# Kernel tuning notes

Hardware: AMD Instinct MI355X
Metric: run time of the kernel (lower is better)

The kernel has to match this reference:

```python
import jax, jax.numpy as jnp
import numpy as np

B, M_IN, M_OUT, C = 4, 16, 32, 32


def setup_inputs() -> dict:
    key = jax.random.key(0)
    kx, = jax.random.split(key, 1)
    x = jax.random.normal(kx, (B, M_IN, C, C, C, C), dtype=jnp.float32)
    init = jnp.ones((M_IN, M_OUT), dtype=jnp.float32) / M_IN
    return {"x": x, "alpha": init, "beta": init, "gamma": init, "delta": init}


def reference(x, alpha, beta, gamma, delta):
    # Faithful to the torch code's permute+sum bookkeeping (note: torch's
    # permute(0,1,3,2,4,5).sum((2,4,5)) reduces ORIGINAL axes (3,4,5),
    # keeping original axis 2 -- identical to s1).
    s1 = x.sum(axis=(3, 4, 5))  # (B, M_in, C), keeps axis 2
    s2 = x.sum(axis=(3, 4, 5))  # same as s1 (permuted-sum in torch keeps axis 2)
    s3 = x.sum(axis=(2, 4, 5))  # keeps axis 3
    s4 = x.sum(axis=(2, 3, 5))  # keeps axis 4
    s = jnp.stack([s1, s2, s3, s4], axis=2)            # (B, M_in, 4, C)
    w = jnp.stack([alpha, beta, gamma, delta], axis=2)  # (M_in, M_out, 4)
    # 'bmic,mnd->bnic': sums over m and w's stack axis d; keeps s's stack axis i.
    out = jnp.einsum('bmic,mnd->bnic', s, w)            # (B, M_out, 4, C)
    return out
```

## Files before the change

kernel.cpp:

```cpp
#include <hip/hip_runtime.h>


__global__ __launch_bounds__(256) void zero_k(float* __restrict__ ws) {
    int i = blockIdx.x * 256 + threadIdx.x;
    if (i < 6144) ws[i] = 0.0f;
}

__global__ __launch_bounds__(256) void reduce_k(const float* __restrict__ x,
                                                float* __restrict__ ws) {
    const int t   = threadIdx.x;
    const int bid = blockIdx.x;
    const int bm  = bid >> 5;
    const int lane = t & 63;
    const int wv   = t >> 6;

    __shared__ float lds3[4][32];
    __shared__ float lds4[32];
    __shared__ float lds1[4];

    const float4* xv = (const float4*)x + (size_t)bid * 8192;

    float total = 0.0f;
    #pragma unroll
    for (int it = 0; it < 32; ++it) {
        float4 v = xv[it * 256 + t];
        float s = (v.x + v.y) + (v.z + v.w);
        total += s;
        #pragma unroll
        for (int off = 1; off < 64; off <<= 1)
            s += __shfl_xor(s, off, 64);
        if (lane == 0) lds3[wv][it] = s;
    }

    float g = total;
    g += __shfl_xor(g, 1, 64);
    g += __shfl_xor(g, 2, 64);
    g += __shfl_xor(g, 4, 64);
    if ((t & 7) == 0) lds4[t >> 3] = g;

    float wsum = g;
    wsum += __shfl_xor(wsum, 8, 64);
    wsum += __shfl_xor(wsum, 16, 64);
    wsum += __shfl_xor(wsum, 32, 64);
    if (lane == 0) lds1[wv] = wsum;

    __syncthreads();

    float* s1 = ws;
    float* s3 = ws + 2048;
    float* s4 = ws + 4096;
    if (t < 32) {
        float v3 = lds3[0][t] + lds3[1][t] + lds3[2][t] + lds3[3][t];
        atomicAdd(&s3[bm * 32 + t], v3);
        atomicAdd(&s4[bm * 32 + t], lds4[t]);
    }
    if (t == 0) {
        s1[bid] = lds1[0] + lds1[1] + lds1[2] + lds1[3];
    }
}

__global__ __launch_bounds__(256) void finalize_k(const float* __restrict__ ws,
                                                  const float* __restrict__ alpha,
                                                  const float* __restrict__ beta,
                                                  const float* __restrict__ gamma,
                                                  const float* __restrict__ delta,
                                                  float* __restrict__ out) {
    __shared__ float W[512];
    const int t = threadIdx.x;
    #pragma unroll
    for (int i = t; i < 512; i += 256)
        W[i] = alpha[i] + beta[i] + gamma[i] + delta[i];
    __syncthreads();

    int gid = blockIdx.x * 256 + t;
    int c  = gid & 31;
    int i4 = (gid >> 5) & 3;
    int n  = (gid >> 7) & 31;
    int b  = gid >> 12;

    const float* s = ws + (i4 <= 1 ? 0 : (i4 == 2 ? 2048 : 4096));
    float acc = 0.0f;
    #pragma unroll
    for (int m = 0; m < 16; ++m)
        acc += s[(b * 16 + m) * 32 + c] * W[m * 32 + n];
    out[gid] = acc;
}

extern "C" void kernel_launch(void* const* d_in, const int* in_sizes, int n_in,
                              void* d_out, int out_size, void* d_ws, size_t ws_size,
                              hipStream_t stream) {
    const float* x     = (const float*)d_in[0];
    const float* alpha = (const float*)d_in[1];
    const float* beta  = (const float*)d_in[2];
    const float* gamma = (const float*)d_in[3];
    const float* delta = (const float*)d_in[4];
    float* out = (float*)d_out;
    float* ws  = (float*)d_ws;

    zero_k<<<24, 256, 0, stream>>>(ws);
    reduce_k<<<2048, 256, 0, stream>>>(x, ws);
    finalize_k<<<64, 256, 0, stream>>>(ws, alpha, beta, gamma, delta, out);
}
```

Baseline: 364.8 us.

## Replace atomics and zero kernel with per-block partials reduced in finalize

The reduce kernel now writes per-block partial sums for s3 and s4 to workspace instead of using atomicAdd into zeroed buffers, so the zeroing kernel launch goes away. The per-lane shuffle tree is cut to three steps, with partials staged through a padded LDS tile. s1 is rebuilt in finalize from the s3 partials. The finalize kernel now runs only 4 blocks that each reduce 32 partials per entry before the contraction, so that final step has much less parallelism.

```diff
diff --git a/kernel.cpp b/kernel.cpp
--- a/kernel.cpp
+++ b/kernel.cpp
@@ -1,89 +1,94 @@
 #include <hip/hip_runtime.h>
 
 
-__global__ __launch_bounds__(256) void zero_k(float* __restrict__ ws) {
-    int i = blockIdx.x * 256 + threadIdx.x;
-    if (i < 6144) ws[i] = 0.0f;
-}
-
 __global__ __launch_bounds__(256) void reduce_k(const float* __restrict__ x,
-                                                float* __restrict__ ws) {
+                                                float* __restrict__ s3part,
+                                                float* __restrict__ s4part) {
     const int t   = threadIdx.x;
     const int bid = blockIdx.x;
-    const int bm  = bid >> 5;
-    const int lane = t & 63;
-    const int wv   = t >> 6;
+    const int wv  = t >> 6;
+    const int g   = (t & 63) >> 3;
 
-    __shared__ float lds3[4][32];
-    __shared__ float lds4[32];
-    __shared__ float lds1[4];
+    __shared__ float lds3[32][33];
 
     const float4* xv = (const float4*)x + (size_t)bid * 8192;
 
-    float total = 0.0f;
-    #pragma unroll
+    float acc4 = 0.0f;
+    #pragma unroll 4
     for (int it = 0; it < 32; ++it) {
         float4 v = xv[it * 256 + t];
         float s = (v.x + v.y) + (v.z + v.w);
-        total += s;
-        #pragma unroll
-        for (int off = 1; off < 64; off <<= 1)
-            s += __shfl_xor(s, off, 64);
-        if (lane == 0) lds3[wv][it] = s;
+        s += __shfl_xor(s, 1, 64);
+        s += __shfl_xor(s, 2, 64);
+        s += __shfl_xor(s, 4, 64);
+        acc4 += s;
+        if ((t & 7) == 0) lds3[it][wv * 8 + g] = s;
     }
 
-    float g = total;
-    g += __shfl_xor(g, 1, 64);
-    g += __shfl_xor(g, 2, 64);
-    g += __shfl_xor(g, 4, 64);
-    if ((t & 7) == 0) lds4[t >> 3] = g;
-
-    float wsum = g;
-    wsum += __shfl_xor(wsum, 8, 64);
-    wsum += __shfl_xor(wsum, 16, 64);
-    wsum += __shfl_xor(wsum, 32, 64);
-    if (lane == 0) lds1[wv] = wsum;
+    if ((t & 7) == 0) s4part[bid * 32 + (t >> 3)] = acc4;
 
     __syncthreads();
 
-    float* s1 = ws;
-    float* s3 = ws + 2048;
-    float* s4 = ws + 4096;
     if (t < 32) {
-        float v3 = lds3[0][t] + lds3[1][t] + lds3[2][t] + lds3[3][t];
-        atomicAdd(&s3[bm * 32 + t], v3);
-        atomicAdd(&s4[bm * 32 + t], lds4[t]);
-    }
-    if (t == 0) {
-        s1[bid] = lds1[0] + lds1[1] + lds1[2] + lds1[3];
+        float a = 0.0f;
+        #pragma unroll
+        for (int k = 0; k < 32; ++k) a += lds3[t][k];
+        s3part[bid * 32 + t] = a;
     }
 }
 
-__global__ __launch_bounds__(256) void finalize_k(const float* __restrict__ ws,
+__global__ __launch_bounds__(256) void finalize_k(const float* __restrict__ s3part,
+                                                  const float* __restrict__ s4part,
                                                   const float* __restrict__ alpha,
                                                   const float* __restrict__ beta,
                                                   const float* __restrict__ gamma,
                                                   const float* __restrict__ delta,
                                                   float* __restrict__ out) {
-    __shared__ float W[512];
+    const int b = blockIdx.x;
     const int t = threadIdx.x;
+
+    __shared__ float S1[16][32];
+    __shared__ float S3[16][32];
+    __shared__ float S4[16][32];
+    __shared__ float W[16][32];
+
     #pragma unroll
     for (int i = t; i < 512; i += 256)
-        W[i] = alpha[i] + beta[i] + gamma[i] + delta[i];
+        W[i >> 5][i & 31] = alpha[i] + beta[i] + gamma[i] + delta[i];
+
+    #pragma unroll
+    for (int idx = t; idx < 512; idx += 256) {
+        const int m = idx >> 5;
+        const int c = idx & 31;
+        const int bm = b * 16 + m;
+        float a3 = 0.0f, a4 = 0.0f;
+        #pragma unroll 4
+        for (int c2 = 0; c2 < 32; ++c2) {
+            a3 += s3part[(bm * 32 + c2) * 32 + c];
+            a4 += s4part[(bm * 32 + c2) * 32 + c];
+        }
+        S3[m][c] = a3;
+        S4[m][c] = a4;
+        float a1 = 0.0f;
+        #pragma unroll 4
+        for (int k = 0; k < 32; ++k)
+            a1 += s3part[(bm * 32 + c) * 32 + k];
+        S1[m][c] = a1;
+    }
     __syncthreads();
 
-    int gid = blockIdx.x * 256 + t;
-    int c  = gid & 31;
-    int i4 = (gid >> 5) & 3;
-    int n  = (gid >> 7) & 31;
-    int b  = gid >> 12;
-
-    const float* s = ws + (i4 <= 1 ? 0 : (i4 == 2 ? 2048 : 4096));
-    float acc = 0.0f;
     #pragma unroll
-    for (int m = 0; m < 16; ++m)
-        acc += s[(b * 16 + m) * 32 + c] * W[m * 32 + n];
-    out[gid] = acc;
+    for (int idx = t; idx < 4096; idx += 256) {
+        const int c = idx & 31;
+        const int i = (idx >> 5) & 3;
+        const int n = idx >> 7;
+        const float (*S)[32] = (i <= 1) ? S1 : (i == 2 ? S3 : S4);
+        float acc = 0.0f;
+        #pragma unroll
+        for (int m = 0; m < 16; ++m)
+            acc += S[m][c] * W[m][n];
+        out[((b * 32 + n) * 4 + i) * 32 + c] = acc;
+    }
 }
 
 extern "C" void kernel_launch(void* const* d_in, const int* in_sizes, int n_in,
@@ -97,7 +102,9 @@
     float* out = (float*)d_out;
     float* ws  = (float*)d_ws;
 
-    zero_k<<<24, 256, 0, stream>>>(ws);
-    reduce_k<<<2048, 256, 0, stream>>>(x, ws);
-    finalize_k<<<64, 256, 0, stream>>>(ws, alpha, beta, gamma, delta, out);
+    float* s3part = ws;
+    float* s4part = ws + 65536;
+
+    reduce_k<<<2048, 256, 0, stream>>>(x, s3part, s4part);
+    finalize_k<<<4, 256, 0, stream>>>(s3part, s4part, alpha, beta, gamma, delta, out);
 }
```

Result: slower. 372.6 us (+2.1%).
